# Performance work log

Hardware: AMD Instinct MI355X
Metric: run time of the kernel (lower is better)

Reference implementation:

```python
import jax, jax.numpy as jnp
import numpy as np

B, DEC, F = 64, 12, 32        # batch, decoder steps, decoder feature size
L, H = 2, 512                 # gru layers, hidden size
E, T = 96, 4                  # encoder seq len, target size


def gru_cell(x, h, Wi, Wh, bi, bh):
    # PyTorch GRUCell math
    gi = x @ Wi.T + bi
    gh = h @ Wh.T + bh
    i_r, i_z, i_n = jnp.split(gi, 3, axis=-1)
    h_r, h_z, h_n = jnp.split(gh, 3, axis=-1)
    r = jax.nn.sigmoid(i_r + h_r)
    z = jax.nn.sigmoid(i_z + h_z)
    n = jnp.tanh(i_n + r * h_n)
    return (1.0 - z) * n + z * h


def setup_inputs() -> dict:
    key = jax.random.key(0)
    ks = jax.random.split(key, 12)
    s = lambda k, shape: jax.random.normal(k, shape, jnp.float32) * 0.02
    return {
        "inputs": jax.random.normal(ks[0], (B, DEC, F), jnp.float32),
        "hidden": jax.random.normal(ks[1], (L, B, H), jnp.float32) * 0.1,
        "enc_outputs": jax.random.normal(ks[2], (B, E, H), jnp.float32),
        "target_indices": jnp.arange(T, dtype=jnp.int32),
        "W_attn": s(ks[3], (H, 2 * H)),
        "b_attn": jnp.zeros((H,), jnp.float32),
        "v_attn": s(ks[4], (H,)),
        "gru_Wi0": s(ks[5], (3 * H, F + H)),
        "gru_Wh0": s(ks[6], (3 * H, H)),
        "gru_bi0": jnp.zeros((3 * H,), jnp.float32),
        "gru_bh0": jnp.zeros((3 * H,), jnp.float32),
        "gru_Wi1": s(ks[7], (3 * H, H)),
        "gru_Wh1": s(ks[8], (3 * H, H)),
        "gru_bi1": jnp.zeros((3 * H,), jnp.float32),
        "gru_bh1": jnp.zeros((3 * H,), jnp.float32),
        "W_out": s(ks[9], (T, 2 * H + F)),
        "b_out": jnp.zeros((T,), jnp.float32),
    }


def reference(inputs, hidden, enc_outputs, target_indices,
              W_attn, b_attn, v_attn,
              gru_Wi0, gru_Wh0, gru_bi0, gru_bh0,
              gru_Wi1, gru_Wh1, gru_bi1, gru_bh1,
              W_out, b_out):
    Hs = hidden.shape[-1]
    Wa_h, Wa_e = W_attn[:, :Hs], W_attn[:, Hs:]
    # encoder projection of the attn linear is constant over timesteps
    enc_proj = jnp.einsum('beh,gh->beg', enc_outputs, Wa_e)  # [B,E,H]
    layers = ((gru_Wi0, gru_Wh0, gru_bi0, gru_bh0),
              (gru_Wi1, gru_Wh1, gru_bi1, gru_bh1))

    def step(carry, x_t):
        h, cur = carry                     # h: [L,B,H], cur: [B,F]
        hl = h[-1]                         # final-layer hidden [B,H]
        energy = jnp.tanh(enc_proj + (hl @ Wa_h.T + b_attn)[:, None, :])
        w = jax.nn.softmax(energy @ v_attn, axis=1)          # [B,E]
        ws = jnp.einsum('be,beh->bh', w, enc_outputs)        # [B,H]
        x = jnp.concatenate([cur, ws], axis=-1)              # [B,F+H]
        new_h = []
        for l, (Wi, Wh, bi, bh) in enumerate(layers):
            hn = gru_cell(x, h[l], Wi, Wh, bi, bh)
            new_h.append(hn)
            x = hn
        out = jnp.concatenate([x, ws, cur], axis=-1) @ W_out.T + b_out  # [B,T]
        nxt = x_t.at[:, target_indices].set(out)  # feed prediction back
        return (jnp.stack(new_h), nxt), out

    xs = jnp.swapaxes(inputs, 0, 1)  # [DEC,B,F]
    (_, _), outs = jax.lax.scan(step, (hidden, inputs[:, 0, :]), xs)
    return jnp.swapaxes(outs, 0, 1)  # [B,DEC,T]
```

## Files before the change

kernel.cpp:

```cpp
#include <hip/hip_runtime.h>
#include <hip/hip_fp16.h>

#define NB   64
#define NDEC 12
#define NF   32
#define NH   512
#define NE   96
#define NT   4
#define KI0  (NF + NH)
#define KOUT (2*NH + NF)

typedef _Float16 half8_t __attribute__((ext_vector_type(8)));
typedef float   float4_t __attribute__((ext_vector_type(4)));

__device__ __forceinline__ float fast_tanh(float x) {
    x = fminf(fmaxf(x, -15.f), 15.f);
    float e = __expf(2.f * x);
    return (e - 1.f) / (e + 1.f);
}
__device__ __forceinline__ float fast_sig(float x) {
    return 1.f / (1.f + __expf(-x));
}

__global__ __launch_bounds__(256) void k_prep(
    const float* __restrict__ Wi0, const float* __restrict__ Wh0,
    const float* __restrict__ Wi1, const float* __restrict__ Wh1,
    const float* __restrict__ Wout, const float* __restrict__ Wattn,
    const float* __restrict__ hidden, const float* __restrict__ inputs,
    __half* __restrict__ Wi0h, __half* __restrict__ Wh0h,
    __half* __restrict__ Wi1h, __half* __restrict__ Wh1h,
    __half* __restrict__ Wouth, __half* __restrict__ WahH,
    __half* __restrict__ WaeH,
    float* __restrict__ h0row, float* __restrict__ h1row,
    __half* __restrict__ h0h, __half* __restrict__ h1h,
    __half* __restrict__ xcat_h)
{
    int i = blockIdx.x*256 + threadIdx.x;
    const int n0 = 1536*KI0, n1 = 1536*512, n4 = 4*KOUT, n5 = 512*512;
    if (i < n0) { Wi0h[i] = __float2half_rn(Wi0[i]); return; }  i -= n0;
    if (i < n1) { Wh0h[i] = __float2half_rn(Wh0[i]); return; }  i -= n1;
    if (i < n1) { Wi1h[i] = __float2half_rn(Wi1[i]); return; }  i -= n1;
    if (i < n1) { Wh1h[i] = __float2half_rn(Wh1[i]); return; }  i -= n1;
    if (i < n4) { Wouth[i] = __float2half_rn(Wout[i]); return; } i -= n4;
    if (i < n5) {
        int g = i >> 9, k = i & 511;
        WahH[i] = __float2half_rn(Wattn[(size_t)g*1024 + k]);
        return;
    }
    i -= n5;
    if (i < n5) {
        int g = i >> 9, k = i & 511;
        WaeH[i] = __float2half_rn(Wattn[(size_t)g*1024 + 512 + k]);
        return;
    }
    i -= n5;
    if (i < NB*NH) {
        int b = i >> 9, k = i & 511;
        float v0 = hidden[b*NH + k];
        float v1 = hidden[NB*NH + b*NH + k];
        h0row[b*NH + k] = v0;  h0h[b*NH + k] = __float2half_rn(v0);
        h1row[b*NH + k] = v1;  h1h[b*NH + k] = __float2half_rn(v1);
        return;
    }
    i -= NB*NH;
    if (i < NB*NF) {
        int b = i >> 5, k = i & 31;
        xcat_h[(size_t)b*KI0 + k] = __float2half_rn(inputs[b*NDEC*NF + k]);
    }
}

__global__ __launch_bounds__(256) void k_encproj(const float* __restrict__ enc,
                                                 const __half* __restrict__ WaeH,
                                                 __half* __restrict__ encph) {
    int x = blockIdx.x;
    int by = x >> 3, bx = x & 7;
    int t = threadIdx.x, w = t >> 6, lane = t & 63;
    int mr = lane & 15, kq = lane >> 4;
    int m = by*64 + w*16 + mr;
    const float* arow = enc + (size_t)m*NH;
    float4_t acc[4] = {{0.f,0.f,0.f,0.f},{0.f,0.f,0.f,0.f},
                       {0.f,0.f,0.f,0.f},{0.f,0.f,0.f,0.f}};
    for (int kb = 0; kb < NH; kb += 32) {
        int k = kb + kq*8;
        float4 a0 = *(const float4*)(arow + k);
        float4 a1 = *(const float4*)(arow + k + 4);
        half8_t a;
        a[0] = (_Float16)a0.x; a[1] = (_Float16)a0.y;
        a[2] = (_Float16)a0.z; a[3] = (_Float16)a0.w;
        a[4] = (_Float16)a1.x; a[5] = (_Float16)a1.y;
        a[6] = (_Float16)a1.z; a[7] = (_Float16)a1.w;
        #pragma unroll
        for (int j = 0; j < 4; ++j) {
            int n = bx*64 + j*16 + mr;
            half8_t b = *(const half8_t*)(WaeH + (size_t)n*NH + k);
            acc[j] = __builtin_amdgcn_mfma_f32_16x16x32_f16(a, b, acc[j], 0, 0, 0);
        }
    }
    #pragma unroll
    for (int j = 0; j < 4; ++j) {
        int col = bx*64 + j*16 + mr;
        #pragma unroll
        for (int r = 0; r < 4; ++r) {
            int row = by*64 + w*16 + kq*4 + r;
            encph[(size_t)row*NH + col] = __float2half_rn(acc[j][r]);
        }
    }
}

__global__ __launch_bounds__(256) void k_gemA(
    const float* __restrict__ inputs, const int* __restrict__ tgt,
    const __half* __restrict__ WahH, const float* __restrict__ battn,
    const __half* __restrict__ Wouth, const float* __restrict__ bout,
    const __half* __restrict__ Wh0h, const __half* __restrict__ Wh1h,
    const __half* __restrict__ h0h, const __half* __restrict__ h1h,
    __half* __restrict__ xcat_h,
    float* __restrict__ attc,
    float* __restrict__ ghb,
    float* __restrict__ out,
    int s, int att_on)
{
    int blk = blockIdx.x, t = threadIdx.x;
    int w = t >> 6, lane = t & 63;
    int mr = lane & 15, kq = lane >> 4;
    int gA = att_on ? 896 : 0;
    __shared__ float parts[4][16][17];

    if (blk < gA) {
        const __half* arow;
        const __half* brow;
        float* dst;
        int is_att, rt16;
        if (blk < 128) {
            int rt = blk >> 2, bq = blk & 3;
            rt16 = rt*16;
            arow = WahH + (size_t)(rt16 + mr)*NH;
            brow = h1h + (size_t)(bq*16 + mr)*NH;
            dst  = attc + (size_t)rt16*NB + bq*16;
            is_att = 1;
        } else {
            int gw = blk - 128;
            int rt = gw >> 2, bq = gw & 3;
            int layer = (rt >= 96) ? 1 : 0;
            int rloc = (rt - layer*96) * 16;
            rt16 = rloc;
            const __half* Wh = layer ? Wh1h : Wh0h;
            const __half* Xh = layer ? h1h : h0h;
            arow = Wh + (size_t)(rloc + mr)*NH;
            brow = Xh + (size_t)(bq*16 + mr)*NH;
            dst  = ghb + ((size_t)layer*3*NH + rloc)*NB + bq*16;
            is_att = 0;
        }
        int kb0 = w*128;
        float4_t acc = {0.f,0.f,0.f,0.f};
        #pragma unroll
        for (int kb = kb0; kb < kb0 + 128; kb += 32) {
            half8_t a = *(const half8_t*)(arow + kb + kq*8);
            half8_t b = *(const half8_t*)(brow + kb + kq*8);
            acc = __builtin_amdgcn_mfma_f32_16x16x32_f16(a, b, acc, 0, 0, 0);
        }
        #pragma unroll
        for (int r = 0; r < 4; ++r) parts[w][kq*4 + r][mr] = acc[r];
        __syncthreads();
        int jl = t >> 4, bl = t & 15;
        float v = parts[0][jl][bl] + parts[1][jl][bl]
                + parts[2][jl][bl] + parts[3][jl][bl];
        if (is_att) v += battn[rt16 + jl];
        dst[(size_t)jl*NB + bl] = v;
        return;
    }

    if (s == 0) return;
    int bq = w;
    int b = bq*16 + mr;
    const __half* h1b = h1h + (size_t)b*NH;
    const __half* xcb = xcat_h + (size_t)b*KI0;
    int ar = (mr < 4) ? mr : 3;
    const __half* arow = Wouth + (size_t)ar*KOUT;
    float4_t acc = {0.f,0.f,0.f,0.f};
    for (int kb = 0; kb < KOUT; kb += 32) {
        int k = kb + kq*8;
        half8_t a = *(const half8_t*)(arow + k);
        const __half* bp = (k < NH)   ? (h1b + k)
                         : (k < 2*NH) ? (xcb + NF + (k - NH))
                                      : (xcb + (k - 2*NH));
        half8_t bb = *(const half8_t*)bp;
        acc = __builtin_amdgcn_mfma_f32_16x16x32_f16(a, bb, acc, 0, 0, 0);
    }
    float o0 = __shfl(acc[0], mr) + bout[0];
    float o1 = __shfl(acc[1], mr) + bout[1];
    float o2 = __shfl(acc[2], mr) + bout[2];
    float o3 = __shfl(acc[3], mr) + bout[3];
    if (kq == 0) {
        *(float4*)(out + (size_t)b*(NDEC*NT) + (s-1)*NT) = make_float4(o0,o1,o2,o3);
    }
    if (s < NDEC) {
        int t0 = tgt[0], t1 = tgt[1], t2 = tgt[2], t3 = tgt[3];
        const float* ip = inputs + (size_t)b*(NDEC*NF) + (s-1)*NF;
        half8_t hv;
        #pragma unroll
        for (int i = 0; i < 8; ++i) {
            int f = kq*8 + i;
            float v = ip[f];
            v = (f == t0) ? o0 : (f == t1) ? o1 : (f == t2) ? o2 : (f == t3) ? o3 : v;
            hv[i] = (_Float16)__float2half_rn(v);
        }
        *(half8_t*)(xcat_h + (size_t)b*KI0 + kq*8) = hv;
    }
}

__global__ __launch_bounds__(1024) void k_soft(
    const float* __restrict__ vattn,
    const float* __restrict__ attc,
    const __half* __restrict__ encph, const float* __restrict__ enc,
    __half* __restrict__ xcat_h)
{
    int b = blockIdx.x, t = threadIdx.x;
    int lane = t & 63, widx = t >> 6;
    __shared__ float vs[NH], atts[NH];
    __shared__ float pes[NE], combA[NH], combB[NH];
    __shared__ float invD_sh;

    if (t < NH) { vs[t] = vattn[t]; atts[t] = attc[(size_t)t*NB + b]; }
    __syncthreads();

    {
        float ar[8], vr[8];
        #pragma unroll
        for (int i = 0; i < 8; ++i) { ar[i] = atts[lane*8 + i]; vr[i] = vs[lane*8 + i]; }
        for (int it = 0; it < 6; ++it) {
            int e = widx + it*16;
            const __half* ep = encph + ((size_t)(b*NE + e))*NH + lane*8;
            uint4 u = *(const uint4*)ep;
            __half2 p0 = *(__half2*)&u.x, p1 = *(__half2*)&u.y;
            __half2 p2 = *(__half2*)&u.z, p3 = *(__half2*)&u.w;
            float2 f0 = __half22float2(p0), f1 = __half22float2(p1);
            float2 f2 = __half22float2(p2), f3 = __half22float2(p3);
            float sacc;
            sacc  = fast_tanh(f0.x + ar[0]) * vr[0];
            sacc += fast_tanh(f0.y + ar[1]) * vr[1];
            sacc += fast_tanh(f1.x + ar[2]) * vr[2];
            sacc += fast_tanh(f1.y + ar[3]) * vr[3];
            sacc += fast_tanh(f2.x + ar[4]) * vr[4];
            sacc += fast_tanh(f2.y + ar[5]) * vr[5];
            sacc += fast_tanh(f3.x + ar[6]) * vr[6];
            sacc += fast_tanh(f3.y + ar[7]) * vr[7];
            #pragma unroll
            for (int off = 32; off; off >>= 1) sacc += __shfl_down(sacc, off);
            if (lane == 0) pes[e] = __expf(sacc);
        }
    }
    __syncthreads();

    if (t < 64) {
        float v = pes[t] + ((t < 32) ? pes[64 + t] : 0.f);
        #pragma unroll
        for (int off = 32; off; off >>= 1) v += __shfl_down(v, off);
        if (t == 0) invD_sh = 1.f / v;
    }
    __syncthreads();

    {
        int k = t & 511, half = t >> 9;
        const float* eb = enc + ((size_t)b*NE + half*48)*NH + k;
        float acc = 0.f;
        #pragma unroll 4
        for (int e = 0; e < 48; ++e) acc += pes[half*48 + e] * eb[(size_t)e*NH];
        if (half == 0) combA[k] = acc; else combB[k] = acc;
    }
    __syncthreads();
    if (t < NH) {
        float v = (combA[t] + combB[t]) * invD_sh;
        xcat_h[(size_t)b*KI0 + NF + t] = __float2half_rn(v);
    }
}

__global__ __launch_bounds__(768) void k_gru(
    const __half* __restrict__ Wi,
    const float* __restrict__ bi, const float* __restrict__ bh,
    const __half* __restrict__ xh, int K,
    const float* __restrict__ ghbL,
    const float* __restrict__ hold,
    float* __restrict__ hnew,
    __half* __restrict__ hnewh)
{
    int blk = blockIdx.x, t = threadIdx.x;
    int w = t >> 6, lane = t & 63;
    int mr = lane & 15, kq = lane >> 4;
    int jg = blk >> 2, bq = blk & 3;
    int j0 = jg*16, b0 = bq*16;
    __shared__ float parts[3][4][16][17];

    int gate = w >> 2, c = w & 3;
    int nsteps = K >> 5;
    int rem = nsteps & 3;
    int base = c*(nsteps >> 2) + ((c < rem) ? c : rem);
    int cnt  = (nsteps >> 2) + ((c < rem) ? 1 : 0);
    const __half* arow = Wi + (size_t)(gate*NH + j0 + mr)*K;
    const __half* brow = xh + (size_t)(b0 + mr)*K;
    float4_t acc = {0.f,0.f,0.f,0.f};
    for (int i2 = 0; i2 < cnt; ++i2) {
        int kb = (base + i2)*32;
        half8_t a = *(const half8_t*)(arow + kb + kq*8);
        half8_t b = *(const half8_t*)(brow + kb + kq*8);
        acc = __builtin_amdgcn_mfma_f32_16x16x32_f16(a, b, acc, 0, 0, 0);
    }
    #pragma unroll
    for (int r = 0; r < 4; ++r) parts[gate][c][kq*4 + r][mr] = acc[r];
    __syncthreads();

    if (t < 256) {
        int jl = t >> 4, bl = t & 15;
        int j = j0 + jl, b = b0 + bl;
        float S0 = parts[0][0][jl][bl] + parts[0][1][jl][bl]
                 + parts[0][2][jl][bl] + parts[0][3][jl][bl];
        float S1 = parts[1][0][jl][bl] + parts[1][1][jl][bl]
                 + parts[1][2][jl][bl] + parts[1][3][jl][bl];
        float S2 = parts[2][0][jl][bl] + parts[2][1][jl][bl]
                 + parts[2][2][jl][bl] + parts[2][3][jl][bl];
        float ghr = ghbL[(size_t)(0*NH + j)*NB + b];
        float ghz = ghbL[(size_t)(1*NH + j)*NB + b];
        float ghn = ghbL[(size_t)(2*NH + j)*NB + b];
        float r = fast_sig(S0 + ghr + bi[j] + bh[j]);
        float z = fast_sig(S1 + ghz + bi[NH + j] + bh[NH + j]);
        float n = fast_tanh(S2 + bi[2*NH + j] + r*(ghn + bh[2*NH + j]));
        float hp = hold[(size_t)b*NH + j];
        float hv = (1.f - z)*n + z*hp;
        hnew[(size_t)b*NH + j] = hv;
        hnewh[(size_t)b*NH + j] = __float2half_rn(hv);
    }
}

extern "C" void kernel_launch(void* const* d_in, const int* in_sizes, int n_in,
                              void* d_out, int out_size, void* d_ws, size_t ws_size,
                              hipStream_t stream) {
    const float* inputs = (const float*)d_in[0];
    const float* hidden = (const float*)d_in[1];
    const float* enc    = (const float*)d_in[2];
    const int*   tgt    = (const int*)d_in[3];
    const float* Wattn  = (const float*)d_in[4];
    const float* battn  = (const float*)d_in[5];
    const float* vattn  = (const float*)d_in[6];
    const float* Wi0    = (const float*)d_in[7];
    const float* Wh0    = (const float*)d_in[8];
    const float* bi0    = (const float*)d_in[9];
    const float* bh0    = (const float*)d_in[10];
    const float* Wi1    = (const float*)d_in[11];
    const float* Wh1    = (const float*)d_in[12];
    const float* bi1    = (const float*)d_in[13];
    const float* bh1    = (const float*)d_in[14];
    const float* Wout   = (const float*)d_in[15];
    const float* bout   = (const float*)d_in[16];
    float* out = (float*)d_out;

    float* h0row  = (float*)d_ws;
    float* h1row  = h0row + NB*NH;
    float* ghb    = h1row + NB*NH;
    float* attc   = ghb + 2*3*NH*NB;
    __half* Wi0h  = (__half*)(attc + NH*NB);
    __half* Wh0h  = Wi0h + 1536*KI0;
    __half* Wi1h  = Wh0h + 1536*NH;
    __half* Wh1h  = Wi1h + 1536*NH;
    __half* Wouth = Wh1h + 1536*NH;
    __half* WahH  = Wouth + 4*KOUT;
    __half* WaeH  = WahH + NH*NH;
    __half* h0h   = WaeH + NH*NH;
    __half* h1h   = h0h + NB*NH;
    __half* xcat_h= h1h + NB*NH;
    __half* encph = xcat_h + NB*KI0;

    const int prep_n = 1536*KI0 + 3*1536*NH + 4*KOUT + 2*NH*NH + NB*NH + NB*NF;
    k_prep<<<(prep_n + 255)/256, 256, 0, stream>>>(
        Wi0, Wh0, Wi1, Wh1, Wout, Wattn, hidden, inputs,
        Wi0h, Wh0h, Wi1h, Wh1h, Wouth, WahH, WaeH,
        h0row, h1row, h0h, h1h, xcat_h);
    k_encproj<<<768, 256, 0, stream>>>(enc, WaeH, encph);

    for (int s = 0; s < NDEC; ++s) {
        k_gemA<<<(s == 0) ? 896 : 897, 256, 0, stream>>>(
            inputs, tgt, WahH, battn, Wouth, bout, Wh0h, Wh1h,
            h0h, h1h, xcat_h, attc, ghb, out, s, 1);
        k_soft<<<NB, 1024, 0, stream>>>(vattn, attc, encph, enc, xcat_h);
        k_gru<<<128, 768, 0, stream>>>(Wi0h, bi0, bh0,
                                       xcat_h, KI0,
                                       ghb,
                                       h0row, h0row, h0h);
        k_gru<<<128, 768, 0, stream>>>(Wi1h, bi1, bh1,
                                       h0h, NH,
                                       ghb + 3*NH*NB,
                                       h1row, h1row, h1h);
    }
    k_gemA<<<1, 256, 0, stream>>>(
        inputs, tgt, WahH, battn, Wouth, bout, Wh0h, Wh1h,
        h0h, h1h, xcat_h, attc, ghb, out, NDEC, 0);
}
```

Baseline: 576.6 us.

## Fuse softmax, both GRU layers and output head into one per-batch kernel

Attention softmax, both GRU input projections, the GRU cell updates and the output projection are merged into a single per-batch kernel launched once per step, replacing three separate kernels plus the output part of the gate kernel. The layer-0 input projection of the attention context is rewritten algebraically: encoder outputs are premultiplied by Wi0 once, and each step combines those rows with the attention weights. This cuts the number of launches per step and removes the xcat round trip through global memory. In exchange, each block re-reads a 96x1536 slice of precomputed fp16 data plus the full transposed Wi1 every step with scalar FMAs on only 64 blocks, so the GPU is heavily underused and weight traffic is no longer shared across the batch.

```diff
diff --git a/kernel.cpp b/kernel.cpp
--- a/kernel.cpp
+++ b/kernel.cpp
@@ -28,18 +28,18 @@
     const float* __restrict__ Wout, const float* __restrict__ Wattn,
     const float* __restrict__ hidden, const float* __restrict__ inputs,
     __half* __restrict__ Wi0h, __half* __restrict__ Wh0h,
-    __half* __restrict__ Wi1h, __half* __restrict__ Wh1h,
-    __half* __restrict__ Wouth, __half* __restrict__ WahH,
-    __half* __restrict__ WaeH,
+    __half* __restrict__ Wh1h, __half* __restrict__ Wouth,
+    __half* __restrict__ WahH, __half* __restrict__ WaeH,
+    __half* __restrict__ Wi0curT,
+    __half* __restrict__ Wi1T2,
     float* __restrict__ h0row, float* __restrict__ h1row,
     __half* __restrict__ h0h, __half* __restrict__ h1h,
-    __half* __restrict__ xcat_h)
+    float* __restrict__ curh)
 {
     int i = blockIdx.x*256 + threadIdx.x;
     const int n0 = 1536*KI0, n1 = 1536*512, n4 = 4*KOUT, n5 = 512*512;
     if (i < n0) { Wi0h[i] = __float2half_rn(Wi0[i]); return; }  i -= n0;
     if (i < n1) { Wh0h[i] = __float2half_rn(Wh0[i]); return; }  i -= n1;
-    if (i < n1) { Wi1h[i] = __float2half_rn(Wi1[i]); return; }  i -= n1;
     if (i < n1) { Wh1h[i] = __float2half_rn(Wh1[i]); return; }  i -= n1;
     if (i < n4) { Wouth[i] = __float2half_rn(Wout[i]); return; } i -= n4;
     if (i < n5) {
@@ -54,6 +54,21 @@
         return;
     }
     i -= n5;
+    if (i < 32*1536) {
+        int k = i / 1536, r = i % 1536;
+        Wi0curT[i] = __float2half_rn(Wi0[(size_t)r*KI0 + k]);
+        return;
+    }
+    i -= 32*1536;
+    if (i < 256*1536) {
+        int kp = i / 1536, r = i % 1536;
+        __half2 v;
+        v.x = __float2half_rn(Wi1[(size_t)r*NH + 2*kp]);
+        v.y = __float2half_rn(Wi1[(size_t)r*NH + 2*kp + 1]);
+        *((__half2*)Wi1T2 + i) = v;
+        return;
+    }
+    i -= 256*1536;
     if (i < NB*NH) {
         int b = i >> 9, k = i & 511;
         float v0 = hidden[b*NH + k];
@@ -65,7 +80,7 @@
     i -= NB*NH;
     if (i < NB*NF) {
         int b = i >> 5, k = i & 31;
-        xcat_h[(size_t)b*KI0 + k] = __float2half_rn(inputs[b*NDEC*NF + k]);
+        curh[b*NF + k] = inputs[b*NDEC*NF + k];
     }
 }
 
@@ -107,120 +122,129 @@
     }
 }
 
+__global__ __launch_bounds__(256) void k_encw(const float* __restrict__ enc,
+                                              const __half* __restrict__ Wi0h,
+                                              __half* __restrict__ encWi0) {
+    int x = blockIdx.x;
+    int by = x / 24, bx = x % 24;
+    int t = threadIdx.x, w = t >> 6, lane = t & 63;
+    int mr = lane & 15, kq = lane >> 4;
+    int m = by*64 + w*16 + mr;
+    const float* arow = enc + (size_t)m*NH;
+    float4_t acc[4] = {{0.f,0.f,0.f,0.f},{0.f,0.f,0.f,0.f},
+                       {0.f,0.f,0.f,0.f},{0.f,0.f,0.f,0.f}};
+    for (int kb = 0; kb < NH; kb += 32) {
+        int k = kb + kq*8;
+        float4 a0 = *(const float4*)(arow + k);
+        float4 a1 = *(const float4*)(arow + k + 4);
+        half8_t a;
+        a[0] = (_Float16)a0.x; a[1] = (_Float16)a0.y;
+        a[2] = (_Float16)a0.z; a[3] = (_Float16)a0.w;
+        a[4] = (_Float16)a1.x; a[5] = (_Float16)a1.y;
+        a[6] = (_Float16)a1.z; a[7] = (_Float16)a1.w;
+        #pragma unroll
+        for (int j = 0; j < 4; ++j) {
+            int n = bx*64 + j*16 + mr;
+            half8_t b = *(const half8_t*)(Wi0h + (size_t)n*KI0 + 32 + k);
+            acc[j] = __builtin_amdgcn_mfma_f32_16x16x32_f16(a, b, acc[j], 0, 0, 0);
+        }
+    }
+    #pragma unroll
+    for (int j = 0; j < 4; ++j) {
+        int col = bx*64 + j*16 + mr;
+        #pragma unroll
+        for (int r = 0; r < 4; ++r) {
+            int row = by*64 + w*16 + kq*4 + r;
+            encWi0[(size_t)row*1536 + col] = __float2half_rn(acc[j][r]);
+        }
+    }
+}
+
 __global__ __launch_bounds__(256) void k_gemA(
-    const float* __restrict__ inputs, const int* __restrict__ tgt,
     const __half* __restrict__ WahH, const float* __restrict__ battn,
-    const __half* __restrict__ Wouth, const float* __restrict__ bout,
     const __half* __restrict__ Wh0h, const __half* __restrict__ Wh1h,
     const __half* __restrict__ h0h, const __half* __restrict__ h1h,
-    __half* __restrict__ xcat_h,
-    float* __restrict__ attc,
-    float* __restrict__ ghb,
-    float* __restrict__ out,
-    int s, int att_on)
+    float* __restrict__ attcT,
+    float* __restrict__ ghbT)
 {
     int blk = blockIdx.x, t = threadIdx.x;
     int w = t >> 6, lane = t & 63;
     int mr = lane & 15, kq = lane >> 4;
-    int gA = att_on ? 896 : 0;
     __shared__ float parts[4][16][17];
 
-    if (blk < gA) {
-        const __half* arow;
-        const __half* brow;
-        float* dst;
-        int is_att, rt16;
-        if (blk < 128) {
-            int rt = blk >> 2, bq = blk & 3;
-            rt16 = rt*16;
-            arow = WahH + (size_t)(rt16 + mr)*NH;
-            brow = h1h + (size_t)(bq*16 + mr)*NH;
-            dst  = attc + (size_t)rt16*NB + bq*16;
-            is_att = 1;
-        } else {
-            int gw = blk - 128;
-            int rt = gw >> 2, bq = gw & 3;
-            int layer = (rt >= 96) ? 1 : 0;
-            int rloc = (rt - layer*96) * 16;
-            rt16 = rloc;
-            const __half* Wh = layer ? Wh1h : Wh0h;
-            const __half* Xh = layer ? h1h : h0h;
-            arow = Wh + (size_t)(rloc + mr)*NH;
-            brow = Xh + (size_t)(bq*16 + mr)*NH;
-            dst  = ghb + ((size_t)layer*3*NH + rloc)*NB + bq*16;
-            is_att = 0;
-        }
-        int kb0 = w*128;
-        float4_t acc = {0.f,0.f,0.f,0.f};
-        #pragma unroll
-        for (int kb = kb0; kb < kb0 + 128; kb += 32) {
-            half8_t a = *(const half8_t*)(arow + kb + kq*8);
-            half8_t b = *(const half8_t*)(brow + kb + kq*8);
-            acc = __builtin_amdgcn_mfma_f32_16x16x32_f16(a, b, acc, 0, 0, 0);
-        }
-        #pragma unroll
-        for (int r = 0; r < 4; ++r) parts[w][kq*4 + r][mr] = acc[r];
-        __syncthreads();
-        int jl = t >> 4, bl = t & 15;
-        float v = parts[0][jl][bl] + parts[1][jl][bl]
-                + parts[2][jl][bl] + parts[3][jl][bl];
-        if (is_att) v += battn[rt16 + jl];
-        dst[(size_t)jl*NB + bl] = v;
-        return;
-    }
-
-    if (s == 0) return;
-    int bq = w;
-    int b = bq*16 + mr;
-    const __half* h1b = h1h + (size_t)b*NH;
-    const __half* xcb = xcat_h + (size_t)b*KI0;
-    int ar = (mr < 4) ? mr : 3;
-    const __half* arow = Wouth + (size_t)ar*KOUT;
+    const __half* arow;
+    const __half* brow;
+    float* dst;
+    int is_att, rt16, b0;
+    if (blk < 128) {
+        int rt = blk >> 2, bq = blk & 3;
+        rt16 = rt*16; b0 = bq*16;
+        arow = WahH + (size_t)(rt16 + mr)*NH;
+        brow = h1h + (size_t)(b0 + mr)*NH;
+        dst  = attcT + (size_t)b0*NH + rt16;
+        is_att = 1;
+    } else {
+        int gw = blk - 128;
+        int rt = gw >> 2, bq = gw & 3;
+        int layer = (rt >= 96) ? 1 : 0;
+        int rloc = (rt - layer*96) * 16;
+        rt16 = rloc; b0 = bq*16;
+        const __half* Wh = layer ? Wh1h : Wh0h;
+        const __half* Xh = layer ? h1h : h0h;
+        arow = Wh + (size_t)(rloc + mr)*NH;
+        brow = Xh + (size_t)(b0 + mr)*NH;
+        dst  = ghbT + (size_t)layer*NB*1536 + (size_t)b0*1536 + rloc;
+        is_att = 0;
+    }
+    int kb0 = w*128;
     float4_t acc = {0.f,0.f,0.f,0.f};
-    for (int kb = 0; kb < KOUT; kb += 32) {
-        int k = kb + kq*8;
-        half8_t a = *(const half8_t*)(arow + k);
-        const __half* bp = (k < NH)   ? (h1b + k)
-                         : (k < 2*NH) ? (xcb + NF + (k - NH))
-                                      : (xcb + (k - 2*NH));
-        half8_t bb = *(const half8_t*)bp;
-        acc = __builtin_amdgcn_mfma_f32_16x16x32_f16(a, bb, acc, 0, 0, 0);
-    }
-    float o0 = __shfl(acc[0], mr) + bout[0];
-    float o1 = __shfl(acc[1], mr) + bout[1];
-    float o2 = __shfl(acc[2], mr) + bout[2];
-    float o3 = __shfl(acc[3], mr) + bout[3];
-    if (kq == 0) {
-        *(float4*)(out + (size_t)b*(NDEC*NT) + (s-1)*NT) = make_float4(o0,o1,o2,o3);
-    }
-    if (s < NDEC) {
-        int t0 = tgt[0], t1 = tgt[1], t2 = tgt[2], t3 = tgt[3];
-        const float* ip = inputs + (size_t)b*(NDEC*NF) + (s-1)*NF;
-        half8_t hv;
-        #pragma unroll
-        for (int i = 0; i < 8; ++i) {
-            int f = kq*8 + i;
-            float v = ip[f];
-            v = (f == t0) ? o0 : (f == t1) ? o1 : (f == t2) ? o2 : (f == t3) ? o3 : v;
-            hv[i] = (_Float16)__float2half_rn(v);
-        }
-        *(half8_t*)(xcat_h + (size_t)b*KI0 + kq*8) = hv;
-    }
-}
-
-__global__ __launch_bounds__(1024) void k_soft(
+    #pragma unroll
+    for (int kb = kb0; kb < kb0 + 128; kb += 32) {
+        half8_t a = *(const half8_t*)(arow + kb + kq*8);
+        half8_t b = *(const half8_t*)(brow + kb + kq*8);
+        acc = __builtin_amdgcn_mfma_f32_16x16x32_f16(a, b, acc, 0, 0, 0);
+    }
+    #pragma unroll
+    for (int r = 0; r < 4; ++r) parts[w][kq*4 + r][mr] = acc[r];
+    __syncthreads();
+    int jl = t & 15, bl = t >> 4;
+    float v = parts[0][jl][bl] + parts[1][jl][bl]
+            + parts[2][jl][bl] + parts[3][jl][bl];
+    if (is_att) v += battn[rt16 + jl];
+    size_t ld = is_att ? NH : 1536;
+    dst[(size_t)bl*ld + jl] = v;
+}
+
+__global__ __launch_bounds__(1024) void k_mega(
+    const float* __restrict__ inputs, const int* __restrict__ tgt,
     const float* __restrict__ vattn,
-    const float* __restrict__ attc,
+    const float* __restrict__ attcT,
+    const float* __restrict__ ghbT,
     const __half* __restrict__ encph, const float* __restrict__ enc,
-    __half* __restrict__ xcat_h)
+    const __half* __restrict__ encWi0,
+    const __half* __restrict__ Wi0curT,
+    const __half* __restrict__ Wi1T2,
+    const float* __restrict__ bi0, const float* __restrict__ bh0,
+    const float* __restrict__ bi1, const float* __restrict__ bh1,
+    const __half* __restrict__ Wouth, const float* __restrict__ bout,
+    float* __restrict__ h0row, float* __restrict__ h1row,
+    __half* __restrict__ h0h, __half* __restrict__ h1h,
+    float* __restrict__ curh,
+    float* __restrict__ out, int s)
 {
     int b = blockIdx.x, t = threadIdx.x;
     int lane = t & 63, widx = t >> 6;
     __shared__ float vs[NH], atts[NH];
-    __shared__ float pes[NE], combA[NH], combB[NH];
+    __shared__ float pes[NE], pws[NE];
+    __shared__ float combA[NH], combB[NH], wsL[NH];
+    __shared__ float curL[NF];
+    __shared__ float sIn[1536];
+    __shared__ float h0n[NH], h1n[NH];
+    __shared__ float outsh[NT];
     __shared__ float invD_sh;
 
-    if (t < NH) { vs[t] = vattn[t]; atts[t] = attc[(size_t)t*NB + b]; }
+    if (t < NH) { vs[t] = vattn[t]; atts[t] = attcT[(size_t)b*NH + t]; }
+    if (t < NF) curL[t] = curh[b*NF + t];
     __syncthreads();
 
     {
@@ -259,6 +283,7 @@
     }
     __syncthreads();
 
+    if (t < NE) pws[t] = pes[t] * invD_sh;
     {
         int k = t & 511, half = t >> 9;
         const float* eb = enc + ((size_t)b*NE + half*48)*NH + k;
@@ -268,65 +293,88 @@
         if (half == 0) combA[k] = acc; else combB[k] = acc;
     }
     __syncthreads();
+    if (t < NH) wsL[t] = (combA[t] + combB[t]) * invD_sh;
+
+    for (int r = t; r < 1536; r += 1024) {
+        float acc = 0.f;
+        const __half* wc = Wi0curT + r;
+        #pragma unroll 8
+        for (int k = 0; k < NF; ++k)
+            acc += curL[k] * __half2float(wc[(size_t)k*1536]);
+        const __half* ew = encWi0 + ((size_t)b*NE)*1536 + r;
+        #pragma unroll 8
+        for (int e = 0; e < NE; ++e)
+            acc += pws[e] * __half2float(ew[(size_t)e*1536]);
+        sIn[r] = acc;
+    }
+    __syncthreads();
+
     if (t < NH) {
-        float v = (combA[t] + combB[t]) * invD_sh;
-        xcat_h[(size_t)b*KI0 + NF + t] = __float2half_rn(v);
-    }
-}
-
-__global__ __launch_bounds__(768) void k_gru(
-    const __half* __restrict__ Wi,
-    const float* __restrict__ bi, const float* __restrict__ bh,
-    const __half* __restrict__ xh, int K,
-    const float* __restrict__ ghbL,
-    const float* __restrict__ hold,
-    float* __restrict__ hnew,
-    __half* __restrict__ hnewh)
-{
-    int blk = blockIdx.x, t = threadIdx.x;
-    int w = t >> 6, lane = t & 63;
-    int mr = lane & 15, kq = lane >> 4;
-    int jg = blk >> 2, bq = blk & 3;
-    int j0 = jg*16, b0 = bq*16;
-    __shared__ float parts[3][4][16][17];
-
-    int gate = w >> 2, c = w & 3;
-    int nsteps = K >> 5;
-    int rem = nsteps & 3;
-    int base = c*(nsteps >> 2) + ((c < rem) ? c : rem);
-    int cnt  = (nsteps >> 2) + ((c < rem) ? 1 : 0);
-    const __half* arow = Wi + (size_t)(gate*NH + j0 + mr)*K;
-    const __half* brow = xh + (size_t)(b0 + mr)*K;
-    float4_t acc = {0.f,0.f,0.f,0.f};
-    for (int i2 = 0; i2 < cnt; ++i2) {
-        int kb = (base + i2)*32;
-        half8_t a = *(const half8_t*)(arow + kb + kq*8);
-        half8_t b = *(const half8_t*)(brow + kb + kq*8);
-        acc = __builtin_amdgcn_mfma_f32_16x16x32_f16(a, b, acc, 0, 0, 0);
-    }
-    #pragma unroll
-    for (int r = 0; r < 4; ++r) parts[gate][c][kq*4 + r][mr] = acc[r];
-    __syncthreads();
-
-    if (t < 256) {
-        int jl = t >> 4, bl = t & 15;
-        int j = j0 + jl, b = b0 + bl;
-        float S0 = parts[0][0][jl][bl] + parts[0][1][jl][bl]
-                 + parts[0][2][jl][bl] + parts[0][3][jl][bl];
-        float S1 = parts[1][0][jl][bl] + parts[1][1][jl][bl]
-                 + parts[1][2][jl][bl] + parts[1][3][jl][bl];
-        float S2 = parts[2][0][jl][bl] + parts[2][1][jl][bl]
-                 + parts[2][2][jl][bl] + parts[2][3][jl][bl];
-        float ghr = ghbL[(size_t)(0*NH + j)*NB + b];
-        float ghz = ghbL[(size_t)(1*NH + j)*NB + b];
-        float ghn = ghbL[(size_t)(2*NH + j)*NB + b];
-        float r = fast_sig(S0 + ghr + bi[j] + bh[j]);
-        float z = fast_sig(S1 + ghz + bi[NH + j] + bh[NH + j]);
-        float n = fast_tanh(S2 + bi[2*NH + j] + r*(ghn + bh[2*NH + j]));
-        float hp = hold[(size_t)b*NH + j];
+        int j = t;
+        const float* g0 = ghbT + (size_t)b*1536;
+        float r_ = fast_sig(sIn[j]        + g0[j]        + bi0[j]        + bh0[j]);
+        float z  = fast_sig(sIn[512 + j]  + g0[512 + j]  + bi0[512 + j]  + bh0[512 + j]);
+        float n  = fast_tanh(sIn[1024 + j] + bi0[1024 + j]
+                             + r_*(g0[1024 + j] + bh0[1024 + j]));
+        float hp = h0row[(size_t)b*NH + j];
         float hv = (1.f - z)*n + z*hp;
-        hnew[(size_t)b*NH + j] = hv;
-        hnewh[(size_t)b*NH + j] = __float2half_rn(hv);
+        h0n[j] = hv;
+        h0row[(size_t)b*NH + j] = hv;
+        h0h[(size_t)b*NH + j] = __float2half_rn(hv);
+    }
+    __syncthreads();
+
+    for (int r = t; r < 1536; r += 1024) {
+        float acc = 0.f;
+        const __half2* wp = (const __half2*)Wi1T2 + r;
+        #pragma unroll 8
+        for (int kp = 0; kp < NH/2; ++kp) {
+            float2 f = __half22float2(wp[(size_t)kp*1536]);
+            acc += f.x*h0n[2*kp] + f.y*h0n[2*kp + 1];
+        }
+        sIn[r] = acc;
+    }
+    __syncthreads();
+
+    if (t < NH) {
+        int j = t;
+        const float* g1 = ghbT + (size_t)NB*1536 + (size_t)b*1536;
+        float r_ = fast_sig(sIn[j]        + g1[j]        + bi1[j]        + bh1[j]);
+        float z  = fast_sig(sIn[512 + j]  + g1[512 + j]  + bi1[512 + j]  + bh1[512 + j]);
+        float n  = fast_tanh(sIn[1024 + j] + bi1[1024 + j]
+                             + r_*(g1[1024 + j] + bh1[1024 + j]));
+        float hp = h1row[(size_t)b*NH + j];
+        float hv = (1.f - z)*n + z*hp;
+        h1n[j] = hv;
+        h1row[(size_t)b*NH + j] = hv;
+        h1h[(size_t)b*NH + j] = __float2half_rn(hv);
+    }
+    __syncthreads();
+
+    if (widx < NT) {
+        const __half* wr = Wouth + (size_t)widx*KOUT;
+        float o = 0.f;
+        for (int c = lane; c < KOUT; c += 64) {
+            float x = (c < NH) ? h1n[c]
+                    : (c < 2*NH ? wsL[c - NH] : curL[c - 2*NH]);
+            o += __half2float(wr[c]) * x;
+        }
+        #pragma unroll
+        for (int off = 32; off; off >>= 1) o += __shfl_down(o, off);
+        if (lane == 0) {
+            o += bout[widx];
+            outsh[widx] = o;
+            out[(size_t)b*(NDEC*NT) + s*NT + widx] = o;
+        }
+    }
+    __syncthreads();
+
+    if (s + 1 < NDEC && t < NF) {
+        float v = inputs[(size_t)b*(NDEC*NF) + s*NF + t];
+        #pragma unroll
+        for (int i = 0; i < NT; ++i)
+            if (t == tgt[i]) v = outsh[i];
+        curh[b*NF + t] = v;
     }
 }
 
@@ -354,42 +402,38 @@
 
     float* h0row  = (float*)d_ws;
     float* h1row  = h0row + NB*NH;
-    float* ghb    = h1row + NB*NH;
-    float* attc   = ghb + 2*3*NH*NB;
-    __half* Wi0h  = (__half*)(attc + NH*NB);
-    __half* Wh0h  = Wi0h + 1536*KI0;
-    __half* Wi1h  = Wh0h + 1536*NH;
-    __half* Wh1h  = Wi1h + 1536*NH;
-    __half* Wouth = Wh1h + 1536*NH;
-    __half* WahH  = Wouth + 4*KOUT;
-    __half* WaeH  = WahH + NH*NH;
-    __half* h0h   = WaeH + NH*NH;
-    __half* h1h   = h0h + NB*NH;
-    __half* xcat_h= h1h + NB*NH;
-    __half* encph = xcat_h + NB*KI0;
-
-    const int prep_n = 1536*KI0 + 3*1536*NH + 4*KOUT + 2*NH*NH + NB*NH + NB*NF;
+    float* ghbT   = h1row + NB*NH;
+    float* attcT  = ghbT + 2*NB*1536;
+    float* curh   = attcT + NB*NH;
+    __half* Wi0h    = (__half*)(curh + NB*NF);
+    __half* Wh0h    = Wi0h + 1536*KI0;
+    __half* Wh1h    = Wh0h + 1536*NH;
+    __half* Wouth   = Wh1h + 1536*NH;
+    __half* WahH    = Wouth + 4*KOUT;
+    __half* WaeH    = WahH + NH*NH;
+    __half* Wi0curT = WaeH + NH*NH;
+    __half* Wi1T2   = Wi0curT + 32*1536;
+    __half* h0h     = Wi1T2 + 2*256*1536;
+    __half* h1h     = h0h + NB*NH;
+    __half* encWi0  = h1h + NB*NH;
+    __half* encph   = encWi0 + (size_t)NB*NE*1536;
+
+    const int prep_n = 1536*KI0 + 2*1536*NH + 4*KOUT + 2*NH*NH
+                     + 32*1536 + 256*1536 + NB*NH + NB*NF;
     k_prep<<<(prep_n + 255)/256, 256, 0, stream>>>(
         Wi0, Wh0, Wi1, Wh1, Wout, Wattn, hidden, inputs,
-        Wi0h, Wh0h, Wi1h, Wh1h, Wouth, WahH, WaeH,
-        h0row, h1row, h0h, h1h, xcat_h);
+        Wi0h, Wh0h, Wh1h, Wouth, WahH, WaeH, Wi0curT, Wi1T2,
+        h0row, h1row, h0h, h1h, curh);
     k_encproj<<<768, 256, 0, stream>>>(enc, WaeH, encph);
+    k_encw<<<2304, 256, 0, stream>>>(enc, Wi0h, encWi0);
 
     for (int s = 0; s < NDEC; ++s) {
-        k_gemA<<<(s == 0) ? 896 : 897, 256, 0, stream>>>(
-            inputs, tgt, WahH, battn, Wouth, bout, Wh0h, Wh1h,
-            h0h, h1h, xcat_h, attc, ghb, out, s, 1);
-        k_soft<<<NB, 1024, 0, stream>>>(vattn, attc, encph, enc, xcat_h);
-        k_gru<<<128, 768, 0, stream>>>(Wi0h, bi0, bh0,
-                                       xcat_h, KI0,
-                                       ghb,
-                                       h0row, h0row, h0h);
-        k_gru<<<128, 768, 0, stream>>>(Wi1h, bi1, bh1,
-                                       h0h, NH,
-                                       ghb + 3*NH*NB,
-                                       h1row, h1row, h1h);
-    }
-    k_gemA<<<1, 256, 0, stream>>>(
-        inputs, tgt, WahH, battn, Wouth, bout, Wh0h, Wh1h,
-        h0h, h1h, xcat_h, attc, ghb, out, NDEC, 0);
-}
+        k_gemA<<<896, 256, 0, stream>>>(
+            WahH, battn, Wh0h, Wh1h, h0h, h1h, attcT, ghbT);
+        k_mega<<<NB, 1024, 0, stream>>>(
+            inputs, tgt, vattn, attcT, ghbT, encph, enc,
+            encWi0, Wi0curT, Wi1T2,
+            bi0, bh0, bi1, bh1, Wouth, bout,
+            h0row, h1row, h0h, h1h, curh, out, s);
+    }
+}
```

New measurement: 1.029 ms. +78.4%, slower.
